# Optimization experiments

Hardware: AMD Instinct MI355X
Metric: run time of the kernel (lower is better)

The kernel has to match this reference:

```python
import jax, jax.numpy as jnp
import numpy as np

N_NODES = 500_000
N_EDGES = 16_000_000
N_LAYERS = 49
ALPHA = 0.3  # GCN2Conv alpha; beta = 1.0 (no theta/layer given)

# per-layer activation applied AFTER the conv (layer index 0-based)
_LEAKY = {1, 11, 21, 31, 41}
_SIG = {4, 14, 24, 34, 44}


def setup_inputs() -> dict:
    key = jax.random.key(0)
    k1, k2, k3 = jax.random.split(key, 3)
    x = jax.random.normal(k1, (N_NODES, 1), dtype=jnp.float32)
    adj = jax.random.randint(k2, (2, N_EDGES), 0, N_NODES, dtype=jnp.int64)
    # 49 scalar (1x1) layer weights
    w = jax.random.normal(k3, (N_LAYERS,), dtype=jnp.float32) * 0.1
    return {"input": x, "w": w, "adj": adj}


def _gcn_norm(adj, n):
    # add self-loops, symmetric normalization D^-1/2 (A+I) D^-1/2
    loops = jnp.arange(n, dtype=adj.dtype)
    src = jnp.concatenate([adj[0], loops])
    dst = jnp.concatenate([adj[1], loops])
    deg = jax.ops.segment_sum(jnp.ones(src.shape[0], jnp.float32), dst, num_segments=n)
    dis = 1.0 / jnp.sqrt(deg)  # deg >= 1 due to self-loops
    ew = dis[src] * dis[dst]
    return src, dst, ew


def reference(input, w, adj):
    n = input.shape[0]
    x0 = input.astype(jnp.float32)
    src, dst, ew = _gcn_norm(adj, n)
    ewc = ew[:, None]  # [E+N, 1]

    def gcn2(x, wl):
        h = jax.ops.segment_sum(ewc * x[src], dst, num_segments=n)  # A_hat @ x
        comb = (1.0 - ALPHA) * h + ALPHA * x0                       # residual mix
        return comb * wl                                            # 1x1 weight, beta=1

    x = x0
    for i in range(N_LAYERS):
        y = gcn2(x, w[i])
        if i == 0:
            x = y  # no activation after gcn1
        elif i == N_LAYERS - 1:
            x = n * jax.nn.sigmoid(y)  # CustomSigmoid: len(x) * sigmoid(x)
        elif i in _LEAKY:
            x = jax.nn.leaky_relu(y, 0.01)
        elif i in _SIG:
            x = jax.nn.sigmoid(y)
        else:
            x = jax.nn.relu(y)
        # dropout(p=0.0) is identity
    return jnp.squeeze(x, 1).astype(jnp.int64)
```

## Files before the change

kernel.cpp:

```cpp
#include <hip/hip_runtime.h>
#include <math.h>

#define NN 500000
#define NE 16000000
#define NBKT 1954
#define PB2 65536
#define NPB2 ((NE + PB2 - 1) / PB2)
#define BKT_CAP 9216

__global__ __launch_bounds__(1024) void hist_kernel(const int4* __restrict__ dst4,
                                                    int* __restrict__ bcnt) {
    __shared__ int lh[NBKT];
    for (int i = threadIdx.x; i < NBKT; i += 1024) lh[i] = 0;
    __syncthreads();
    long base4 = (long)blockIdx.x * (PB2 / 4);
    for (int k = 0; k < PB2 / 4; k += 1024) {
        long i4 = base4 + k + threadIdx.x;
        if (i4 < NE / 4) {
            int4 d = dst4[i4];
            atomicAdd(&lh[d.x >> 8], 1);
            atomicAdd(&lh[d.y >> 8], 1);
            atomicAdd(&lh[d.z >> 8], 1);
            atomicAdd(&lh[d.w >> 8], 1);
        }
    }
    __syncthreads();
    for (int i = threadIdx.x; i < NBKT; i += 1024) {
        int c = lh[i];
        if (c) atomicAdd(&bcnt[i], c);
    }
}

__global__ __launch_bounds__(256) void scan_buckets(int* __restrict__ bcnt,
                                                    int* __restrict__ bbase) {
    __shared__ int sh[256];
    __shared__ int carry_sh;
    if (threadIdx.x == 0) carry_sh = 0;
    __syncthreads();
    for (int base = 0; base < NBKT; base += 256) {
        int i = base + threadIdx.x;
        int v = (i < NBKT) ? bcnt[i] : 0;
        sh[threadIdx.x] = v;
        __syncthreads();
        for (int off = 1; off < 256; off <<= 1) {
            int t = (threadIdx.x >= off) ? sh[threadIdx.x - off] : 0;
            __syncthreads();
            sh[threadIdx.x] += t;
            __syncthreads();
        }
        int incl = sh[threadIdx.x];
        int c = carry_sh;
        __syncthreads();
        if (i < NBKT) {
            int ex = c + incl - v;
            bbase[i] = ex;
            bcnt[i] = ex;
        }
        if (threadIdx.x == 255) carry_sh = c + incl;
        __syncthreads();
    }
    if (threadIdx.x == 0) bbase[NBKT] = NE;
}

__global__ __launch_bounds__(1024) void partition_kernel(const int4* __restrict__ src4,
                                                         const int4* __restrict__ dst4,
                                                         int* __restrict__ bcur,
                                                         int* __restrict__ ebuf) {
    __shared__ int lh[NBKT];
    for (int i = threadIdx.x; i < NBKT; i += 1024) lh[i] = 0;
    __syncthreads();
    long base4 = (long)blockIdx.x * (PB2 / 4);
    for (int k = 0; k < PB2 / 4; k += 1024) {
        long i4 = base4 + k + threadIdx.x;
        if (i4 < NE / 4) {
            int4 d = dst4[i4];
            atomicAdd(&lh[d.x >> 8], 1);
            atomicAdd(&lh[d.y >> 8], 1);
            atomicAdd(&lh[d.z >> 8], 1);
            atomicAdd(&lh[d.w >> 8], 1);
        }
    }
    __syncthreads();
    for (int i = threadIdx.x; i < NBKT; i += 1024) {
        int c = lh[i];
        if (c) lh[i] = atomicAdd(&bcur[i], c);
    }
    __syncthreads();
    for (int k = 0; k < PB2 / 4; k += 1024) {
        long i4 = base4 + k + threadIdx.x;
        if (i4 < NE / 4) {
            int4 d = dst4[i4];
            int4 s = src4[i4];
            int pos;
            pos = atomicAdd(&lh[d.x >> 8], 1); ebuf[pos] = ((d.x & 255) << 19) | s.x;
            pos = atomicAdd(&lh[d.y >> 8], 1); ebuf[pos] = ((d.y & 255) << 19) | s.y;
            pos = atomicAdd(&lh[d.z >> 8], 1); ebuf[pos] = ((d.z & 255) << 19) | s.z;
            pos = atomicAdd(&lh[d.w >> 8], 1); ebuf[pos] = ((d.w & 255) << 19) | s.w;
        }
    }
}

__global__ __launch_bounds__(256) void bucket_csr(const int* __restrict__ bbase,
                                                  int* __restrict__ ebuf,
                                                  int* __restrict__ rp,
                                                  float* __restrict__ dis) {
    __shared__ int eds[BKT_CAP];
    __shared__ int outb[BKT_CAP];
    __shared__ int cnt[256];
    __shared__ int scn[256];
    int b = blockIdx.x;
    int ebase = bbase[b];
    int nb = bbase[b + 1] - ebase;
    if (nb > BKT_CAP) nb = BKT_CAP;
    for (int i = threadIdx.x; i < nb; i += 256) eds[i] = ebuf[ebase + i];
    cnt[threadIdx.x] = 0;
    __syncthreads();
    for (int i = threadIdx.x; i < nb; i += 256) atomicAdd(&cnt[eds[i] >> 19], 1);
    __syncthreads();
    int my = cnt[threadIdx.x];
    scn[threadIdx.x] = my;
    __syncthreads();
    for (int off = 1; off < 256; off <<= 1) {
        int t = (threadIdx.x >= off) ? scn[threadIdx.x - off] : 0;
        __syncthreads();
        scn[threadIdx.x] += t;
        __syncthreads();
    }
    int excl = scn[threadIdx.x] - my;
    int v = b * 256 + threadIdx.x;
    if (v < NN) {
        rp[v] = ebase + excl;
        dis[v] = rsqrtf((float)(my + 1));
    }
    __syncthreads();
    cnt[threadIdx.x] = excl;
    __syncthreads();
    for (int i = threadIdx.x; i < nb; i += 256) {
        int p = eds[i];
        int pos = atomicAdd(&cnt[p >> 19], 1);
        outb[pos] = p & 0x7FFFF;
    }
    __syncthreads();
    for (int i = threadIdx.x; i < nb; i += 256) ebuf[ebase + i] = outb[i];
    if (b == 0 && threadIdx.x == 0) rp[NN] = NE;
}

__global__ void init_z(const float* __restrict__ x0, const float* __restrict__ dis,
                       float* __restrict__ z) {
    int i = blockIdx.x * 256 + threadIdx.x;
    if (i < NN) z[i] = x0[i] * dis[i];
}

__global__ __launch_bounds__(256) void layer_kernel(
        const int* __restrict__ rp, const int* __restrict__ csr,
        const float* __restrict__ zin, const float* __restrict__ dis,
        const float* __restrict__ x0, const float* __restrict__ w,
        int li, int act, float* __restrict__ zout, int* __restrict__ out) {
    int tid = blockIdx.x * 256 + threadIdx.x;
    int v = tid >> 3;
    int lane = threadIdx.x & 7;
    int beg = rp[v];
    int end = rp[v + 1];
    float s = 0.f;
    int j = beg + lane;
    for (; j + 24 < end; j += 32) {
        int c0 = csr[j];
        int c1 = csr[j + 8];
        int c2 = csr[j + 16];
        int c3 = csr[j + 24];
        float z0 = zin[c0];
        float z1 = zin[c1];
        float z2 = zin[c2];
        float z3 = zin[c3];
        s += z0; s += z1; s += z2; s += z3;
    }
    for (; j < end; j += 8) s += zin[csr[j]];
    s += __shfl_xor(s, 1);
    s += __shfl_xor(s, 2);
    s += __shfl_xor(s, 4);
    if (lane != 0) return;
    s += zin[v];
    float h = dis[v] * s;
    float comb = 0.7f * h + 0.3f * x0[v];
    float y = comb * w[li];
    if (act == 4) {
        float sg = 1.f / (1.f + expf(-y));
        out[v] = (int)(500000.f * sg);
        return;
    }
    float r;
    if (act == 0)      r = y;
    else if (act == 1) r = fmaxf(y, 0.f);
    else if (act == 2) r = (y > 0.f) ? y : 0.01f * y;
    else               r = 1.f / (1.f + expf(-y));
    zout[v] = dis[v] * r;
}

extern "C" void kernel_launch(void* const* d_in, const int* in_sizes, int n_in,
                              void* d_out, int out_size, void* d_ws, size_t ws_size,
                              hipStream_t stream) {
    const float* x0  = (const float*)d_in[0];
    const float* w   = (const float*)d_in[1];
    const int*   adj = (const int*)d_in[2];
    const int*   src = adj;
    const int*   dst = adj + NE;
    int* out = (int*)d_out;

    uintptr_t p = (uintptr_t)d_ws;
    auto alloc = [&](size_t bytes) -> void* {
        p = (p + 255) & ~(uintptr_t)255;
        void* r = (void*)p;
        p += bytes;
        return r;
    };
    float* dis   = (float*)alloc((size_t)NN * 4);
    int*   rp    = (int*)alloc((size_t)(NN + 1) * 4);
    float* z0    = (float*)alloc((size_t)NN * 4);
    float* z1    = (float*)alloc((size_t)NN * 4);
    int*   bcnt  = (int*)alloc((size_t)NBKT * 4);
    int*   bbase = (int*)alloc((size_t)(NBKT + 1) * 4);
    int*   csr   = (int*)alloc((size_t)NE * 4);
    (void)ws_size;

    hipMemsetAsync(bcnt, 0, (size_t)NBKT * 4, stream);

    hist_kernel<<<NPB2, 1024, 0, stream>>>((const int4*)dst, bcnt);
    scan_buckets<<<1, 256, 0, stream>>>(bcnt, bbase);
    partition_kernel<<<NPB2, 1024, 0, stream>>>((const int4*)src, (const int4*)dst, bcnt, csr);
    bucket_csr<<<NBKT, 256, 0, stream>>>(bbase, csr, rp, dis);
    init_z<<<(NN + 255) / 256, 256, 0, stream>>>(x0, dis, z0);

    float* zbuf[2] = {z0, z1};
    const int LB = (NN * 8) / 256;
    for (int i = 0; i < 49; i++) {
        int act;
        if (i == 0)            act = 0;
        else if (i == 48)      act = 4;
        else if (i % 10 == 1)  act = 2;
        else if (i % 10 == 4)  act = 3;
        else                   act = 1;
        layer_kernel<<<LB, 256, 0, stream>>>(rp, csr, zbuf[i & 1], dis, x0, w,
                                             i, act, zbuf[(i + 1) & 1], out);
    }
}
```

Baseline: 4.091 ms.

## Widen CSR buckets to 512 nodes, fuse z init, use relaxed atomic gathers

New measurement: 4.054 ms. Within noise of the previous version (-0.9%).

```diff
diff --git a/kernel.cpp b/kernel.cpp
--- a/kernel.cpp
+++ b/kernel.cpp
@@ -3,10 +3,11 @@
 
 #define NN 500000
 #define NE 16000000
-#define NBKT 1954
+#define BSH 9
+#define NBKT 977
 #define PB2 65536
 #define NPB2 ((NE + PB2 - 1) / PB2)
-#define BKT_CAP 9216
+#define BKT_CAP 17920
 
 __global__ __launch_bounds__(1024) void hist_kernel(const int4* __restrict__ dst4,
                                                     int* __restrict__ bcnt) {
@@ -18,10 +19,10 @@
         long i4 = base4 + k + threadIdx.x;
         if (i4 < NE / 4) {
             int4 d = dst4[i4];
-            atomicAdd(&lh[d.x >> 8], 1);
-            atomicAdd(&lh[d.y >> 8], 1);
-            atomicAdd(&lh[d.z >> 8], 1);
-            atomicAdd(&lh[d.w >> 8], 1);
+            atomicAdd(&lh[d.x >> BSH], 1);
+            atomicAdd(&lh[d.y >> BSH], 1);
+            atomicAdd(&lh[d.z >> BSH], 1);
+            atomicAdd(&lh[d.w >> BSH], 1);
         }
     }
     __syncthreads();
@@ -74,10 +75,10 @@
         long i4 = base4 + k + threadIdx.x;
         if (i4 < NE / 4) {
             int4 d = dst4[i4];
-            atomicAdd(&lh[d.x >> 8], 1);
-            atomicAdd(&lh[d.y >> 8], 1);
-            atomicAdd(&lh[d.z >> 8], 1);
-            atomicAdd(&lh[d.w >> 8], 1);
+            atomicAdd(&lh[d.x >> BSH], 1);
+            atomicAdd(&lh[d.y >> BSH], 1);
+            atomicAdd(&lh[d.z >> BSH], 1);
+            atomicAdd(&lh[d.w >> BSH], 1);
         }
     }
     __syncthreads();
@@ -92,63 +93,61 @@
             int4 d = dst4[i4];
             int4 s = src4[i4];
             int pos;
-            pos = atomicAdd(&lh[d.x >> 8], 1); ebuf[pos] = ((d.x & 255) << 19) | s.x;
-            pos = atomicAdd(&lh[d.y >> 8], 1); ebuf[pos] = ((d.y & 255) << 19) | s.y;
-            pos = atomicAdd(&lh[d.z >> 8], 1); ebuf[pos] = ((d.z & 255) << 19) | s.z;
-            pos = atomicAdd(&lh[d.w >> 8], 1); ebuf[pos] = ((d.w & 255) << 19) | s.w;
-        }
-    }
-}
-
-__global__ __launch_bounds__(256) void bucket_csr(const int* __restrict__ bbase,
+            pos = atomicAdd(&lh[d.x >> BSH], 1); ebuf[pos] = ((d.x & 511) << 19) | s.x;
+            pos = atomicAdd(&lh[d.y >> BSH], 1); ebuf[pos] = ((d.y & 511) << 19) | s.y;
+            pos = atomicAdd(&lh[d.z >> BSH], 1); ebuf[pos] = ((d.z & 511) << 19) | s.z;
+            pos = atomicAdd(&lh[d.w >> BSH], 1); ebuf[pos] = ((d.w & 511) << 19) | s.w;
+        }
+    }
+}
+
+__global__ __launch_bounds__(512) void bucket_csr(const int* __restrict__ bbase,
                                                   int* __restrict__ ebuf,
                                                   int* __restrict__ rp,
-                                                  float* __restrict__ dis) {
+                                                  float* __restrict__ dis,
+                                                  const float* __restrict__ x0,
+                                                  float* __restrict__ z0) {
     __shared__ int eds[BKT_CAP];
     __shared__ int outb[BKT_CAP];
-    __shared__ int cnt[256];
-    __shared__ int scn[256];
+    __shared__ int cnt[512];
+    __shared__ int scn[512];
     int b = blockIdx.x;
     int ebase = bbase[b];
     int nb = bbase[b + 1] - ebase;
     if (nb > BKT_CAP) nb = BKT_CAP;
-    for (int i = threadIdx.x; i < nb; i += 256) eds[i] = ebuf[ebase + i];
+    for (int i = threadIdx.x; i < nb; i += 512) eds[i] = ebuf[ebase + i];
     cnt[threadIdx.x] = 0;
     __syncthreads();
-    for (int i = threadIdx.x; i < nb; i += 256) atomicAdd(&cnt[eds[i] >> 19], 1);
+    for (int i = threadIdx.x; i < nb; i += 512) atomicAdd(&cnt[eds[i] >> 19], 1);
     __syncthreads();
     int my = cnt[threadIdx.x];
     scn[threadIdx.x] = my;
     __syncthreads();
-    for (int off = 1; off < 256; off <<= 1) {
+    for (int off = 1; off < 512; off <<= 1) {
         int t = (threadIdx.x >= off) ? scn[threadIdx.x - off] : 0;
         __syncthreads();
         scn[threadIdx.x] += t;
         __syncthreads();
     }
     int excl = scn[threadIdx.x] - my;
-    int v = b * 256 + threadIdx.x;
+    int v = b * 512 + threadIdx.x;
     if (v < NN) {
         rp[v] = ebase + excl;
-        dis[v] = rsqrtf((float)(my + 1));
+        float dv = rsqrtf((float)(my + 1));
+        dis[v] = dv;
+        z0[v] = x0[v] * dv;
     }
     __syncthreads();
     cnt[threadIdx.x] = excl;
     __syncthreads();
-    for (int i = threadIdx.x; i < nb; i += 256) {
+    for (int i = threadIdx.x; i < nb; i += 512) {
         int p = eds[i];
         int pos = atomicAdd(&cnt[p >> 19], 1);
         outb[pos] = p & 0x7FFFF;
     }
     __syncthreads();
-    for (int i = threadIdx.x; i < nb; i += 256) ebuf[ebase + i] = outb[i];
+    for (int i = threadIdx.x; i < nb; i += 512) ebuf[ebase + i] = outb[i];
     if (b == 0 && threadIdx.x == 0) rp[NN] = NE;
-}
-
-__global__ void init_z(const float* __restrict__ x0, const float* __restrict__ dis,
-                       float* __restrict__ z) {
-    int i = blockIdx.x * 256 + threadIdx.x;
-    if (i < NN) z[i] = x0[i] * dis[i];
 }
 
 __global__ __launch_bounds__(256) void layer_kernel(
@@ -168,13 +167,14 @@
         int c1 = csr[j + 8];
         int c2 = csr[j + 16];
         int c3 = csr[j + 24];
-        float z0 = zin[c0];
-        float z1 = zin[c1];
-        float z2 = zin[c2];
-        float z3 = zin[c3];
+        float z0 = __hip_atomic_load(&zin[c0], __ATOMIC_RELAXED, __HIP_MEMORY_SCOPE_AGENT);
+        float z1 = __hip_atomic_load(&zin[c1], __ATOMIC_RELAXED, __HIP_MEMORY_SCOPE_AGENT);
+        float z2 = __hip_atomic_load(&zin[c2], __ATOMIC_RELAXED, __HIP_MEMORY_SCOPE_AGENT);
+        float z3 = __hip_atomic_load(&zin[c3], __ATOMIC_RELAXED, __HIP_MEMORY_SCOPE_AGENT);
         s += z0; s += z1; s += z2; s += z3;
     }
-    for (; j < end; j += 8) s += zin[csr[j]];
+    for (; j < end; j += 8)
+        s += __hip_atomic_load(&zin[csr[j]], __ATOMIC_RELAXED, __HIP_MEMORY_SCOPE_AGENT);
     s += __shfl_xor(s, 1);
     s += __shfl_xor(s, 2);
     s += __shfl_xor(s, 4);
@@ -227,8 +227,7 @@
     hist_kernel<<<NPB2, 1024, 0, stream>>>((const int4*)dst, bcnt);
     scan_buckets<<<1, 256, 0, stream>>>(bcnt, bbase);
     partition_kernel<<<NPB2, 1024, 0, stream>>>((const int4*)src, (const int4*)dst, bcnt, csr);
-    bucket_csr<<<NBKT, 256, 0, stream>>>(bbase, csr, rp, dis);
-    init_z<<<(NN + 255) / 256, 256, 0, stream>>>(x0, dis, z0);
+    bucket_csr<<<NBKT, 512, 0, stream>>>(bbase, csr, rp, dis, x0, z0);
 
     float* zbuf[2] = {z0, z1};
     const int LB = (NN * 8) / 256;
```
